# Kernel optimization log

Hardware: AMD Instinct MI355X
Metric: run time of the kernel (lower is better)

Reference implementation:

```python
import jax, jax.numpy as jnp
import numpy as np

T, B, D, H = 2048, 4, 1024, 16
HD = D // H  # head_dim = 64


def setup_inputs() -> dict:
    key = jax.random.key(0)
    ks = jax.random.split(key, 12)
    s = 1.0 / np.sqrt(D)
    return {
        "query": jax.random.normal(ks[0], (T, B, D), jnp.float32),
        "key": jax.random.normal(ks[1], (T, B, D), jnp.float32),
        "value": jax.random.normal(ks[2], (T, B, D), jnp.float32),
        "time_decay": jax.random.uniform(ks[3], (T, B, D), jnp.float32),
        "Wq": jax.random.normal(ks[4], (D, D), jnp.float32) * s,
        "bq": jax.random.normal(ks[5], (D,), jnp.float32) * s,
        "Wk": jax.random.normal(ks[6], (D, D), jnp.float32) * s,
        "bk": jax.random.normal(ks[7], (D,), jnp.float32) * s,
        "Wv": jax.random.normal(ks[8], (D, D), jnp.float32) * s,
        "bv": jax.random.normal(ks[9], (D,), jnp.float32) * s,
        "Wo": jax.random.normal(ks[10], (D, D), jnp.float32) * s,
        "bo": jax.random.normal(ks[11], (D,), jnp.float32) * s,
    }


def reference(query, key, value, time_decay, Wq, bq, Wk, bk, Wv, bv, Wo, bo):
    # Linear projections (torch Linear: x @ W.T + b). Inputs are (T, B, D).
    def split_heads(x, W, b):
        y = x @ W.T + b  # (T, B, D)
        # -> (B, H, T, HD)
        return y.reshape(T, B, H, HD).transpose(1, 2, 0, 3)

    Q = split_heads(query, Wq, bq)
    K = split_heads(key, Wk, bk)
    V = split_heads(value, Wv, bv)

    scale = 1.0 / np.sqrt(HD)
    scores = jnp.einsum("bhqd,bhkd->bhqk", Q, K) * scale  # (B, H, T, T)
    attn = jax.nn.softmax(scores, axis=-1)
    ctx = jnp.einsum("bhqk,bhkd->bhqd", attn, V)  # (B, H, T, HD)
    # -> (T, B, D)
    ctx = ctx.transpose(2, 0, 1, 3).reshape(T, B, D)
    out = ctx @ Wo.T + bo
    return out * time_decay
```

## Files before the change

### kernel.cpp

```cpp
#include <hip/hip_runtime.h>

#define TT 2048
#define BB 4
#define DD 1024
#define HH 16
#define HDIM 64
#define MM (TT*BB)

typedef __attribute__((ext_vector_type(4))) float float4v;
typedef _Float16 half8 __attribute__((ext_vector_type(8)));
typedef _Float16 half4 __attribute__((ext_vector_type(4)));
typedef _Float16 half2v __attribute__((ext_vector_type(2)));

static __device__ __forceinline__ half4 pk4(float a, float b, float c, float d) {
    half2v h0 = __builtin_bit_cast(half2v, __builtin_amdgcn_cvt_pkrtz(a, b));
    half2v h1 = __builtin_bit_cast(half2v, __builtin_amdgcn_cvt_pkrtz(c, d));
    half4 hv; hv[0]=h0[0]; hv[1]=h0[1]; hv[2]=h1[0]; hv[3]=h1[1];
    return hv;
}

static __device__ __forceinline__ float fexp2(float x) {
    float r; asm("v_exp_f32 %0, %1" : "=v"(r) : "v"(x)); return r;
}

#define GLD16(g, l) __builtin_amdgcn_global_load_lds( \
    (const __attribute__((address_space(1))) unsigned int*)(g), \
    (__attribute__((address_space(3))) unsigned int*)(l), 16, 0, 0)

__global__ __launch_bounds__(256) void cvt_f16(
    const float* __restrict__ q, const float* __restrict__ k, const float* __restrict__ v,
    const float* __restrict__ wq, const float* __restrict__ wk, const float* __restrict__ wv,
    const float* __restrict__ wo,
    _Float16* __restrict__ qh, _Float16* __restrict__ kh, _Float16* __restrict__ vh,
    _Float16* __restrict__ wqh, _Float16* __restrict__ wkh, _Float16* __restrict__ wvh,
    _Float16* __restrict__ woh)
{
    const int z = blockIdx.z;
    const float* src; _Float16* dst; int n;
    switch (z) {
        case 0: src=q;  dst=qh;  n=MM*DD/8; break;
        case 1: src=k;  dst=kh;  n=MM*DD/8; break;
        case 2: src=v;  dst=vh;  n=MM*DD/8; break;
        case 3: src=wq; dst=wqh; n=DD*DD/8; break;
        case 4: src=wk; dst=wkh; n=DD*DD/8; break;
        case 5: src=wv; dst=wvh; n=DD*DD/8; break;
        default: src=wo; dst=woh; n=DD*DD/8; break;
    }
    for (int c = blockIdx.x*blockDim.x + threadIdx.x; c < n; c += gridDim.x*blockDim.x) {
        const float4v* s4 = (const float4v*)src + (size_t)c*2;
        float4v a = s4[0], b = s4[1];
        *(half4*)(dst + (size_t)c*8)     = pk4(a[0],a[1],a[2],a[3]);
        *(half4*)(dst + (size_t)c*8 + 4) = pk4(b[0],b[1],b[2],b[3]);
    }
}

__global__ __launch_bounds__(256) void qkv_gemm(
    const _Float16* __restrict__ xq, const _Float16* __restrict__ xk, const _Float16* __restrict__ xv,
    const _Float16* __restrict__ wqh, const _Float16* __restrict__ wkh, const _Float16* __restrict__ wvh,
    const float* __restrict__ bq, const float* __restrict__ bk, const float* __restrict__ bv,
    _Float16* __restrict__ dq, _Float16* __restrict__ dk, _Float16* __restrict__ dv)
{
    const int z = blockIdx.z;
    const _Float16* X = (z==0)?xq:((z==1)?xk:xv);
    const _Float16* W = (z==0)?wqh:((z==1)?wkh:wvh);
    const float* Bb   = (z==0)?bq:((z==1)?bk:bv);
    _Float16* Dst     = (z==0)?dq:((z==1)?dk:dv);
    const float osc   = (z==0) ? 0.18033688011112042f : 1.0f;

    __shared__ __attribute__((aligned(16))) _Float16 As[128*64];
    __shared__ __attribute__((aligned(16))) _Float16 Bs[128*64];

    const int tid=threadIdx.x, lane=tid&63, w=tid>>6;
    const int wm=w>>1, wn=w&1;
    const int m0=blockIdx.y*128, n0=blockIdx.x*128;
    const int lrow=lane&15, lg=lane>>4;

    const _Float16* ga = X + (size_t)(m0 + w*32 + (lane>>3))*DD + (lane&7)*8;
    const _Float16* gb = W + (size_t)(n0 + w*32 + (lane>>3))*DD + (lane&7)*8;
    _Float16* la = As + (w*32)*64;
    _Float16* lb = Bs + (w*32)*64;

    float4v acc[4][4];
    for (int i=0;i<4;i++) for (int j=0;j<4;j++) acc[i][j]=(float4v){0.f,0.f,0.f,0.f};

    for (int k0=0;k0<DD;k0+=64) {
        __syncthreads();
        #pragma unroll
        for (int s=0;s<4;s++) GLD16(ga + (size_t)s*8*DD + k0, la + s*8*64);
        #pragma unroll
        for (int s=0;s<4;s++) GLD16(gb + (size_t)s*8*DD + k0, lb + s*8*64);
        __syncthreads();
        #pragma unroll
        for (int kc=0;kc<2;kc++) {
            half8 a[4], b[4];
            #pragma unroll
            for (int i=0;i<4;i++) a[i] = *(const half8*)&As[(wm*64+i*16+lrow)*64 + kc*32 + lg*8];
            #pragma unroll
            for (int j=0;j<4;j++) b[j] = *(const half8*)&Bs[(wn*64+j*16+lrow)*64 + kc*32 + lg*8];
            #pragma unroll
            for (int i=0;i<4;i++)
            #pragma unroll
            for (int j=0;j<4;j++)
                acc[i][j] = __builtin_amdgcn_mfma_f32_16x16x32_f16(a[i], b[j], acc[i][j],0,0,0);
        }
    }
    #pragma unroll
    for (int j=0;j<4;j++) {
        int n = n0 + wn*64 + j*16 + lrow;
        float bias = Bb[n];
        int h = n >> 6, hd = n & 63;
        #pragma unroll
        for (int i=0;i<4;i++)
        #pragma unroll
        for (int r=0;r<4;r++) {
            int m = m0 + wm*64 + i*16 + lg*4 + r;
            int t = m >> 2, b = m & 3;
            Dst[((size_t)(b*HH + h)*TT + t)*HDIM + hd] = (_Float16)((acc[i][j][r] + bias)*osc);
        }
    }
}

__global__ __launch_bounds__(256) void v_transpose(
    const _Float16* __restrict__ Vb, _Float16* __restrict__ VbT)
{
    const int tile = blockIdx.x;
    const int bh   = blockIdx.y;
    const int tid = threadIdx.x, tg = tid & 15, hg = tid >> 4;
    const int t0 = tile*64;

    half4 rv[4];
    #pragma unroll
    for (int r=0;r<4;r++)
        rv[r] = *(const half4*)(Vb + ((size_t)bh*TT + t0 + tg*4 + r)*HDIM + hg*4);
    #pragma unroll
    for (int c=0;c<4;c++) {
        half4 tv; tv[0]=rv[0][c]; tv[1]=rv[1][c]; tv[2]=rv[2][c]; tv[3]=rv[3][c];
        *(half4*)(VbT + ((size_t)bh*HDIM + hg*4 + c)*TT + t0 + tg*4) = tv;
    }
}

__global__ __launch_bounds__(256, 4) void attn(
    const _Float16* __restrict__ Qg, const _Float16* __restrict__ Kg,
    const _Float16* __restrict__ VT, _Float16* __restrict__ Ctx)
{
    __shared__ __attribute__((aligned(16))) _Float16 Kt[2][64*64];
    __shared__ __attribute__((aligned(16))) _Float16 Vs[2][64*64];

    const int id = blockIdx.x;
    const int bh = id & 63, qt = id >> 6;
    const int b = bh >> 4, h = bh & 15;
    const int tid = threadIdx.x, lane = tid & 63, w = tid >> 6;
    const int lrow = lane & 15, lg = lane >> 4;

    const _Float16* Qb  = Qg + ((size_t)bh*TT + qt*128)*HDIM;
    const _Float16* Kb  = Kg + (size_t)bh*TT*HDIM;
    const _Float16* Vtb = VT + (size_t)bh*HDIM*TT;

    const int srow = w*16 + (lane>>3);
    const int scol = ((lane&7) ^ (lane>>3))*8;

    half8 qf[2][2];
    #pragma unroll
    for (int i=0;i<2;i++)
    #pragma unroll
    for (int kc=0;kc<2;kc++)
        qf[i][kc] = *(const half8*)(Qb + (size_t)(w*32 + i*16 + lrow)*HDIM + kc*32 + lg*8);

    float4v oacc[2][4];
    for (int i=0;i<2;i++) for (int j=0;j<4;j++) oacc[i][j]=(float4v){0.f,0.f,0.f,0.f};
    float lsum[2] = {0.f, 0.f};

    #pragma unroll
    for (int s=0;s<2;s++) {
        GLD16(Kb  + (size_t)(srow + s*8)*HDIM + scol,        &Kt[0][(w*16 + s*8)*64]);
        GLD16(Vtb + (size_t)(srow + s*8)*TT   + scol,        &Vs[0][(w*16 + s*8)*64]);
    }
    __syncthreads();

    const int swz = (lrow & 7) << 3;

    for (int kt = 0; kt < 32; kt++) {
        const int cb = kt & 1, nb = cb ^ 1;

        if (kt < 31) {
            #pragma unroll
            for (int s=0;s<2;s++) {
                GLD16(Kb  + (size_t)((kt+1)*64 + srow + s*8)*HDIM + scol, &Kt[nb][(w*16 + s*8)*64]);
                GLD16(Vtb + (size_t)(srow + s*8)*TT + (kt+1)*64 + scol,   &Vs[nb][(w*16 + s*8)*64]);
            }
        }

        float4v st[4][2];
        #pragma unroll
        for (int j=0;j<4;j++) for (int i=0;i<2;i++) st[j][i]=(float4v){0.f,0.f,0.f,0.f};
        #pragma unroll
        for (int kc=0;kc<2;kc++) {
            half8 kf[4];
            #pragma unroll
            for (int j=0;j<4;j++)
                kf[j] = *(const half8*)&Kt[cb][(j*16 + lrow)*64 + ((kc*32 + lg*8) ^ swz)];
            __builtin_amdgcn_s_setprio(1);
            #pragma unroll
            for (int j=0;j<4;j++)
            #pragma unroll
            for (int i=0;i<2;i++)
                st[j][i] = __builtin_amdgcn_mfma_f32_16x16x32_f16(kf[j], qf[i][kc], st[j][i],0,0,0);
            __builtin_amdgcn_s_setprio(0);
        }

        #pragma unroll
        for (int j=0;j<4;j++) {
            half4 pa[2];
            #pragma unroll
            for (int i=0;i<2;i++) {
                float p0 = fexp2(st[j][i][0]);
                float p1 = fexp2(st[j][i][1]);
                float p2 = fexp2(st[j][i][2]);
                float p3 = fexp2(st[j][i][3]);
                lsum[i] += (p0+p1)+(p2+p3);
                pa[i] = pk4(p0,p1,p2,p3);
            }
            half4 vf[4];
            #pragma unroll
            for (int jo=0;jo<4;jo++)
                vf[jo] = *(const half4*)&Vs[cb][(jo*16 + lrow)*64 + ((j*16 + lg*4) ^ swz)];
            __builtin_amdgcn_s_setprio(1);
            #pragma unroll
            for (int i=0;i<2;i++)
            #pragma unroll
            for (int jo=0;jo<4;jo++)
                oacc[i][jo] = __builtin_amdgcn_mfma_f32_16x16x16f16(vf[jo], pa[i], oacc[i][jo],0,0,0);
            __builtin_amdgcn_s_setprio(0);
        }

        __syncthreads();
    }

    #pragma unroll
    for (int i=0;i<2;i++) {
        float s = lsum[i];
        s += __shfl_xor(s, 16, 64);
        s += __shfl_xor(s, 32, 64);
        lsum[i] = s;
    }

    #pragma unroll
    for (int i=0;i<2;i++) {
        float inv = 1.f / lsum[i];
        int t = qt*128 + w*32 + i*16 + lrow;
        _Float16* crow = Ctx + ((size_t)t*BB + b)*DD + h*HDIM;
        #pragma unroll
        for (int jo=0;jo<4;jo++) {
            *(half4*)(crow + jo*16 + lg*4) =
                pk4(oacc[i][jo][0]*inv, oacc[i][jo][1]*inv,
                    oacc[i][jo][2]*inv, oacc[i][jo][3]*inv);
        }
    }
}

__global__ __launch_bounds__(256) void out_gemm(
    const _Float16* __restrict__ Cx, const _Float16* __restrict__ Woh,
    const float* __restrict__ bo, const float* __restrict__ td,
    float* __restrict__ Out)
{
    __shared__ __attribute__((aligned(16))) _Float16 As[128*64];
    __shared__ __attribute__((aligned(16))) _Float16 Bs[128*64];

    const int tid=threadIdx.x, lane=tid&63, w=tid>>6;
    const int wm=w>>1, wn=w&1;
    const int m0=blockIdx.y*128, n0=blockIdx.x*128;
    const int lrow=lane&15, lg=lane>>4;

    const _Float16* ga = Cx  + (size_t)(m0 + w*32 + (lane>>3))*DD + (lane&7)*8;
    const _Float16* gb = Woh + (size_t)(n0 + w*32 + (lane>>3))*DD + (lane&7)*8;
    _Float16* la = As + (w*32)*64;
    _Float16* lb = Bs + (w*32)*64;

    float4v acc[4][4];
    for (int i=0;i<4;i++) for (int j=0;j<4;j++) acc[i][j]=(float4v){0.f,0.f,0.f,0.f};

    for (int k0=0;k0<DD;k0+=64) {
        __syncthreads();
        #pragma unroll
        for (int s=0;s<4;s++) GLD16(ga + (size_t)s*8*DD + k0, la + s*8*64);
        #pragma unroll
        for (int s=0;s<4;s++) GLD16(gb + (size_t)s*8*DD + k0, lb + s*8*64);
        __syncthreads();
        #pragma unroll
        for (int kc=0;kc<2;kc++) {
            half8 a[4], b[4];
            #pragma unroll
            for (int i=0;i<4;i++) a[i] = *(const half8*)&As[(wm*64+i*16+lrow)*64 + kc*32 + lg*8];
            #pragma unroll
            for (int j=0;j<4;j++) b[j] = *(const half8*)&Bs[(wn*64+j*16+lrow)*64 + kc*32 + lg*8];
            #pragma unroll
            for (int i=0;i<4;i++)
            #pragma unroll
            for (int j=0;j<4;j++)
                acc[i][j] = __builtin_amdgcn_mfma_f32_16x16x32_f16(a[i], b[j], acc[i][j],0,0,0);
        }
    }
    #pragma unroll
    for (int j=0;j<4;j++) {
        int n = n0 + wn*64 + j*16 + lrow;
        float bias = bo[n];
        #pragma unroll
        for (int i=0;i<4;i++)
        #pragma unroll
        for (int r=0;r<4;r++) {
            int m = m0 + wm*64 + i*16 + lg*4 + r;
            size_t off = (size_t)m*DD + n;
            Out[off] = (acc[i][j][r] + bias) * td[off];
        }
    }
}

extern "C" void kernel_launch(void* const* d_in, const int* in_sizes, int n_in,
                              void* d_out, int out_size, void* d_ws, size_t ws_size,
                              hipStream_t stream) {
    const float* q  = (const float*)d_in[0];
    const float* k  = (const float*)d_in[1];
    const float* v  = (const float*)d_in[2];
    const float* td = (const float*)d_in[3];
    const float* Wq = (const float*)d_in[4];
    const float* bq = (const float*)d_in[5];
    const float* Wk = (const float*)d_in[6];
    const float* bk = (const float*)d_in[7];
    const float* Wv = (const float*)d_in[8];
    const float* bv = (const float*)d_in[9];
    const float* Wo = (const float*)d_in[10];
    const float* bo = (const float*)d_in[11];
    float* out = (float*)d_out;

    _Float16* qh  = (_Float16*)d_ws;
    _Float16* kh  = qh  + (size_t)MM*DD;
    _Float16* vh  = kh  + (size_t)MM*DD;
    _Float16* wqh = vh  + (size_t)MM*DD;
    _Float16* wkh = wqh + (size_t)DD*DD;
    _Float16* wvh = wkh + (size_t)DD*DD;
    _Float16* woh = wvh + (size_t)DD*DD;
    _Float16* Qb  = woh + (size_t)DD*DD;
    _Float16* Kb  = Qb  + (size_t)MM*DD;
    _Float16* Vb  = Kb  + (size_t)MM*DD;
    _Float16* VbT = vh;
    _Float16* Cx  = qh;

    cvt_f16    <<<dim3(2048,1,7), 256, 0, stream>>>(q,k,v, Wq,Wk,Wv,Wo, qh,kh,vh, wqh,wkh,wvh,woh);
    qkv_gemm   <<<dim3(8,64,3),   256, 0, stream>>>(qh,kh,vh, wqh,wkh,wvh, bq,bk,bv, Qb,Kb,Vb);
    v_transpose<<<dim3(32,64),    256, 0, stream>>>(Vb, VbT);
    attn       <<<dim3(1024),     256, 0, stream>>>(Qb, Kb, VbT, Cx);
    out_gemm   <<<dim3(8,64),     256, 0, stream>>>(Cx, woh, bo, td, out);
}
```

Measured before the change: 394.1 us.

## Double-buffer LDS, XOR-swizzle tiles, and remap blocks across XCDs in projection GEMMs

Both projection GEMMs now use two LDS buffers so the global-to-LDS load of the next K tile overlaps MFMA work on the current one, with one barrier per iteration instead of two. The LDS column index is XOR-swizzled by row to reduce bank conflicts on the half8 fragment reads. Grids are flattened to 1D and block ids are remapped so consecutive tiles land on the same XCD for better L2 reuse. The QKV kernel relies on the three fp16 weight matrices being contiguous in the workspace, and the doubled LDS footprint (64 KB per block) may lower occupancy.

Measured after the change: 371.5 us. 5.7% less time.

```diff
diff --git a/kernel.cpp b/kernel.cpp
--- a/kernel.cpp
+++ b/kernel.cpp
@@ -56,57 +56,71 @@
 
 __global__ __launch_bounds__(256) void qkv_gemm(
     const _Float16* __restrict__ xq, const _Float16* __restrict__ xk, const _Float16* __restrict__ xv,
-    const _Float16* __restrict__ wqh, const _Float16* __restrict__ wkh, const _Float16* __restrict__ wvh,
+    const _Float16* __restrict__ wall,
     const float* __restrict__ bq, const float* __restrict__ bk, const float* __restrict__ bv,
     _Float16* __restrict__ dq, _Float16* __restrict__ dk, _Float16* __restrict__ dv)
 {
-    const int z = blockIdx.z;
+    __shared__ __attribute__((aligned(16))) _Float16 As[2][128*64];
+    __shared__ __attribute__((aligned(16))) _Float16 Bs[2][128*64];
+
+    const int id   = blockIdx.x;
+    const int wgid = (id & 7)*192 + (id >> 3);
+    const int z    = wgid / 512;
+    const int rem  = wgid & 511;
+    const int by   = rem >> 3, bx = rem & 7;
+    const int m0   = by*128, n0l = bx*128;
+
     const _Float16* X = (z==0)?xq:((z==1)?xk:xv);
-    const _Float16* W = (z==0)?wqh:((z==1)?wkh:wvh);
     const float* Bb   = (z==0)?bq:((z==1)?bk:bv);
     _Float16* Dst     = (z==0)?dq:((z==1)?dk:dv);
     const float osc   = (z==0) ? 0.18033688011112042f : 1.0f;
 
-    __shared__ __attribute__((aligned(16))) _Float16 As[128*64];
-    __shared__ __attribute__((aligned(16))) _Float16 Bs[128*64];
-
     const int tid=threadIdx.x, lane=tid&63, w=tid>>6;
     const int wm=w>>1, wn=w&1;
-    const int m0=blockIdx.y*128, n0=blockIdx.x*128;
     const int lrow=lane&15, lg=lane>>4;
-
-    const _Float16* ga = X + (size_t)(m0 + w*32 + (lane>>3))*DD + (lane&7)*8;
-    const _Float16* gb = W + (size_t)(n0 + w*32 + (lane>>3))*DD + (lane&7)*8;
-    _Float16* la = As + (w*32)*64;
-    _Float16* lb = Bs + (w*32)*64;
+    const int swzr = (lrow & 7) << 3;
+
+    const int scol = ((lane&7) ^ (lane>>3))*8;
+    const _Float16* ga = X    + (size_t)(m0 + w*32 + (lane>>3))*DD + scol;
+    const _Float16* gb = wall + (size_t)(z*1024 + n0l + w*32 + (lane>>3))*DD + scol;
 
     float4v acc[4][4];
     for (int i=0;i<4;i++) for (int j=0;j<4;j++) acc[i][j]=(float4v){0.f,0.f,0.f,0.f};
 
-    for (int k0=0;k0<DD;k0+=64) {
-        __syncthreads();
-        #pragma unroll
-        for (int s=0;s<4;s++) GLD16(ga + (size_t)s*8*DD + k0, la + s*8*64);
-        #pragma unroll
-        for (int s=0;s<4;s++) GLD16(gb + (size_t)s*8*DD + k0, lb + s*8*64);
-        __syncthreads();
+    #pragma unroll
+    for (int s=0;s<4;s++) GLD16(ga + (size_t)s*8*DD, &As[0][(w*32+s*8)*64]);
+    #pragma unroll
+    for (int s=0;s<4;s++) GLD16(gb + (size_t)s*8*DD, &Bs[0][(w*32+s*8)*64]);
+    __syncthreads();
+
+    for (int t=0; t<16; t++) {
+        const int cb = t & 1, nb = cb ^ 1;
+        if (t < 15) {
+            const size_t k1 = (size_t)(t+1)*64;
+            #pragma unroll
+            for (int s=0;s<4;s++) GLD16(ga + (size_t)s*8*DD + k1, &As[nb][(w*32+s*8)*64]);
+            #pragma unroll
+            for (int s=0;s<4;s++) GLD16(gb + (size_t)s*8*DD + k1, &Bs[nb][(w*32+s*8)*64]);
+        }
         #pragma unroll
         for (int kc=0;kc<2;kc++) {
             half8 a[4], b[4];
             #pragma unroll
-            for (int i=0;i<4;i++) a[i] = *(const half8*)&As[(wm*64+i*16+lrow)*64 + kc*32 + lg*8];
-            #pragma unroll
-            for (int j=0;j<4;j++) b[j] = *(const half8*)&Bs[(wn*64+j*16+lrow)*64 + kc*32 + lg*8];
+            for (int i=0;i<4;i++) a[i] = *(const half8*)&As[cb][(wm*64+i*16+lrow)*64 + ((kc*32+lg*8) ^ swzr)];
+            #pragma unroll
+            for (int j=0;j<4;j++) b[j] = *(const half8*)&Bs[cb][(wn*64+j*16+lrow)*64 + ((kc*32+lg*8) ^ swzr)];
             #pragma unroll
             for (int i=0;i<4;i++)
             #pragma unroll
             for (int j=0;j<4;j++)
                 acc[i][j] = __builtin_amdgcn_mfma_f32_16x16x32_f16(a[i], b[j], acc[i][j],0,0,0);
         }
-    }
+        __syncthreads();
+    }
+
     #pragma unroll
     for (int j=0;j<4;j++) {
-        int n = n0 + wn*64 + j*16 + lrow;
+        int n = n0l + wn*64 + j*16 + lrow;
         float bias = Bb[n];
         int h = n >> 6, hd = n & 63;
         #pragma unroll
@@ -114,8 +128,8 @@
         #pragma unroll
         for (int r=0;r<4;r++) {
             int m = m0 + wm*64 + i*16 + lg*4 + r;
-            int t = m >> 2, b = m & 3;
-            Dst[((size_t)(b*HH + h)*TT + t)*HDIM + hd] = (_Float16)((acc[i][j][r] + bias)*osc);
+            int tt = m >> 2, b = m & 3;
+            Dst[((size_t)(b*HH + h)*TT + tt)*HDIM + hd] = (_Float16)((acc[i][j][r] + bias)*osc);
         }
     }
 }
@@ -263,43 +277,57 @@
     const float* __restrict__ bo, const float* __restrict__ td,
     float* __restrict__ Out)
 {
-    __shared__ __attribute__((aligned(16))) _Float16 As[128*64];
-    __shared__ __attribute__((aligned(16))) _Float16 Bs[128*64];
+    __shared__ __attribute__((aligned(16))) _Float16 As[2][128*64];
+    __shared__ __attribute__((aligned(16))) _Float16 Bs[2][128*64];
+
+    const int id   = blockIdx.x;
+    const int wgid = (id & 7)*64 + (id >> 3);
+    const int by   = wgid >> 3, bx = wgid & 7;
+    const int m0   = by*128, n0 = bx*128;
 
     const int tid=threadIdx.x, lane=tid&63, w=tid>>6;
     const int wm=w>>1, wn=w&1;
-    const int m0=blockIdx.y*128, n0=blockIdx.x*128;
     const int lrow=lane&15, lg=lane>>4;
-
-    const _Float16* ga = Cx  + (size_t)(m0 + w*32 + (lane>>3))*DD + (lane&7)*8;
-    const _Float16* gb = Woh + (size_t)(n0 + w*32 + (lane>>3))*DD + (lane&7)*8;
-    _Float16* la = As + (w*32)*64;
-    _Float16* lb = Bs + (w*32)*64;
+    const int swzr = (lrow & 7) << 3;
+
+    const int scol = ((lane&7) ^ (lane>>3))*8;
+    const _Float16* ga = Cx  + (size_t)(m0 + w*32 + (lane>>3))*DD + scol;
+    const _Float16* gb = Woh + (size_t)(n0 + w*32 + (lane>>3))*DD + scol;
 
     float4v acc[4][4];
     for (int i=0;i<4;i++) for (int j=0;j<4;j++) acc[i][j]=(float4v){0.f,0.f,0.f,0.f};
 
-    for (int k0=0;k0<DD;k0+=64) {
-        __syncthreads();
-        #pragma unroll
-        for (int s=0;s<4;s++) GLD16(ga + (size_t)s*8*DD + k0, la + s*8*64);
-        #pragma unroll
-        for (int s=0;s<4;s++) GLD16(gb + (size_t)s*8*DD + k0, lb + s*8*64);
-        __syncthreads();
+    #pragma unroll
+    for (int s=0;s<4;s++) GLD16(ga + (size_t)s*8*DD, &As[0][(w*32+s*8)*64]);
+    #pragma unroll
+    for (int s=0;s<4;s++) GLD16(gb + (size_t)s*8*DD, &Bs[0][(w*32+s*8)*64]);
+    __syncthreads();
+
+    for (int t=0; t<16; t++) {
+        const int cb = t & 1, nb = cb ^ 1;
+        if (t < 15) {
+            const size_t k1 = (size_t)(t+1)*64;
+            #pragma unroll
+            for (int s=0;s<4;s++) GLD16(ga + (size_t)s*8*DD + k1, &As[nb][(w*32+s*8)*64]);
+            #pragma unroll
+            for (int s=0;s<4;s++) GLD16(gb + (size_t)s*8*DD + k1, &Bs[nb][(w*32+s*8)*64]);
+        }
         #pragma unroll
         for (int kc=0;kc<2;kc++) {
             half8 a[4], b[4];
             #pragma unroll
-            for (int i=0;i<4;i++) a[i] = *(const half8*)&As[(wm*64+i*16+lrow)*64 + kc*32 + lg*8];
-            #pragma unroll
-            for (int j=0;j<4;j++) b[j] = *(const half8*)&Bs[(wn*64+j*16+lrow)*64 + kc*32 + lg*8];
+            for (int i=0;i<4;i++) a[i] = *(const half8*)&As[cb][(wm*64+i*16+lrow)*64 + ((kc*32+lg*8) ^ swzr)];
+            #pragma unroll
+            for (int j=0;j<4;j++) b[j] = *(const half8*)&Bs[cb][(wn*64+j*16+lrow)*64 + ((kc*32+lg*8) ^ swzr)];
             #pragma unroll
             for (int i=0;i<4;i++)
             #pragma unroll
             for (int j=0;j<4;j++)
                 acc[i][j] = __builtin_amdgcn_mfma_f32_16x16x32_f16(a[i], b[j], acc[i][j],0,0,0);
         }
-    }
+        __syncthreads();
+    }
+
     #pragma unroll
     for (int j=0;j<4;j++) {
         int n = n0 + wn*64 + j*16 + lrow;
@@ -346,8 +374,8 @@
     _Float16* Cx  = qh;
 
     cvt_f16    <<<dim3(2048,1,7), 256, 0, stream>>>(q,k,v, Wq,Wk,Wv,Wo, qh,kh,vh, wqh,wkh,wvh,woh);
-    qkv_gemm   <<<dim3(8,64,3),   256, 0, stream>>>(qh,kh,vh, wqh,wkh,wvh, bq,bk,bv, Qb,Kb,Vb);
+    qkv_gemm   <<<dim3(1536),     256, 0, stream>>>(qh,kh,vh, wqh, bq,bk,bv, Qb,Kb,Vb);
     v_transpose<<<dim3(32,64),    256, 0, stream>>>(Vb, VbT);
     attn       <<<dim3(1024),     256, 0, stream>>>(Qb, Kb, VbT, Cx);
-    out_gemm   <<<dim3(8,64),     256, 0, stream>>>(Cx, woh, bo, td, out);
-}
+    out_gemm   <<<dim3(512),      256, 0, stream>>>(Cx, woh, bo, td, out);
+}
```
